# Performance work log

Measured on AMD Instinct MI355X. Metric: run time of the kernel, lower is better.

Reference implementation:

```python
import jax, jax.numpy as jnp
import numpy as np

N_NODES = 100000
N_EDGES = 625000
D = 128
N_LAYERS = 10

def setup_inputs() -> dict:
    key = jax.random.key(0)
    ks = jax.random.split(key, 6)
    x = jax.random.normal(ks[0], (N_NODES, D), dtype=jnp.float32)
    edge_index = jax.random.randint(ks[1], (2, N_EDGES), 0, N_NODES, dtype=jnp.int32)
    # PyG SAGEConv params per layer: lin_l (aggregated msgs, with bias), lin_r (root, no bias)
    scale = 1.0 / np.sqrt(D)
    Wl = jax.random.normal(ks[2], (N_LAYERS, D, D), dtype=jnp.float32) * scale
    Wr = jax.random.normal(ks[3], (N_LAYERS, D, D), dtype=jnp.float32) * scale
    b = jax.random.normal(ks[4], (N_LAYERS, D), dtype=jnp.float32) * 0.01
    return {"x": x, "Wl": Wl, "Wr": Wr, "b": b, "edge_index": edge_index}

def reference(x, Wl, Wr, b, edge_index):
    src = edge_index[0]
    dst = edge_index[1]
    n = x.shape[0]
    # in-degree for mean aggregation (clamped to avoid div by zero)
    deg = jax.ops.segment_sum(jnp.ones(src.shape[0], x.dtype), dst, num_segments=n)
    deg = jnp.maximum(deg, 1.0)[:, None]
    n_layers = Wl.shape[0]
    for i in range(n_layers):
        # SAGEConv: out = lin_l(mean_{j in N(i)} x_j) + lin_r(x_i)
        agg = jax.ops.segment_sum(x[src], dst, num_segments=n) / deg
        x = agg @ Wl[i] + x @ Wr[i] + b[i]
        if i < n_layers - 1:
            x = jax.nn.relu(x)  # dropout is identity in eval mode
    return x
```

## Files before the change

### kernel.cpp

```cpp
#include <hip/hip_runtime.h>
#include <hip/hip_bf16.h>

#define N_NODES 100000
#define N_EDGES 625000
#define D 128
#define N_LAYERS 10
#define SCAN_BLOCKS 98

typedef __attribute__((ext_vector_type(8))) short bf16x8;
typedef __attribute__((ext_vector_type(4))) float floatx4;

static __device__ __forceinline__ ushort f2bf(float f) {
    uint u = __float_as_uint(f);
    u += 0x7fff + ((u >> 16) & 1);
    return (ushort)(u >> 16);
}
static __device__ __forceinline__ float bf2f(ushort h) {
    return __uint_as_float(((uint)h) << 16);
}
static __device__ __forceinline__ uint packbf(float lo, float hi) {
    return (uint)f2bf(lo) | ((uint)f2bf(hi) << 16);
}


__global__ void hist_kernel(const int* __restrict__ dst, int* __restrict__ deg) {
    int e = blockIdx.x * blockDim.x + threadIdx.x;
    if (e < N_EDGES) atomicAdd(&deg[dst[e]], 1);
}

__global__ void scanA_kernel(const int* __restrict__ deg, int* __restrict__ offsets,
                             int* __restrict__ blockSums) {
    __shared__ int s[1024];
    int tid = threadIdx.x;
    int i = blockIdx.x * 1024 + tid;
    int v = (i < N_NODES) ? deg[i] : 0;
    s[tid] = v;
    __syncthreads();
    for (int d = 1; d < 1024; d <<= 1) {
        int t = (tid >= d) ? s[tid - d] : 0;
        __syncthreads();
        s[tid] += t;
        __syncthreads();
    }
    if (i < N_NODES) offsets[i] = s[tid] - v;
    if (tid == 1023) blockSums[blockIdx.x] = s[1023];
}

__global__ void scanB_kernel(const int* __restrict__ blockSums, int* __restrict__ blockOffsets) {
    __shared__ int s[128];
    int tid = threadIdx.x;
    int v = (tid < SCAN_BLOCKS) ? blockSums[tid] : 0;
    s[tid] = v;
    __syncthreads();
    for (int d = 1; d < 128; d <<= 1) {
        int t = (tid >= d) ? s[tid - d] : 0;
        __syncthreads();
        s[tid] += t;
        __syncthreads();
    }
    blockOffsets[tid] = s[tid] - v;
}

__global__ void scanC_kernel(int* __restrict__ offsets, const int* __restrict__ blockOffsets) {
    int i = blockIdx.x * 1024 + threadIdx.x;
    if (i < N_NODES) offsets[i] += blockOffsets[blockIdx.x];
}

__global__ void invdeg_kernel(const int* __restrict__ deg, float* __restrict__ invdeg,
                              int* __restrict__ offsets) {
    int i = blockIdx.x * blockDim.x + threadIdx.x;
    if (i < N_NODES) {
        int d = deg[i];
        invdeg[i] = 1.0f / (float)(d > 0 ? d : 1);
    }
    if (i == 0) offsets[N_NODES] = N_EDGES;
}

__global__ void scatter_kernel(const int* __restrict__ src, const int* __restrict__ dst,
                               const int* __restrict__ offsets, int* __restrict__ fill,
                               int* __restrict__ srcSorted) {
    int e = blockIdx.x * blockDim.x + threadIdx.x;
    if (e < N_EDGES) {
        int d_ = dst[e];
        int pos = offsets[d_] + atomicAdd(&fill[d_], 1);
        srcSorted[pos] = src[e];
    }
}

__global__ void wsplit_kernel(const float* __restrict__ Wl, const float* __restrict__ Wr,
                              ushort* __restrict__ Whi, ushort* __restrict__ Wlo) {
    int t = blockIdx.x * blockDim.x + threadIdx.x;
    if (t >= N_LAYERS * 4 * 16 * 64) return;
    int lane  = t & 63;
    int ntile = (t >> 6) & 15;
    int s     = (t >> 10) & 3;
    int layer = t >> 12;
    int n = ntile * 16 + (lane & 15);
    int kbase = s * 32 + (lane >> 4) * 8;
    const float* W = (n < 128) ? (Wl + (size_t)layer * D * D + n)
                               : (Wr + (size_t)layer * D * D + (n - 128));
    size_t off = (size_t)t * 8;
#pragma unroll
    for (int j = 0; j < 8; ++j) {
        float w = W[(size_t)(kbase + j) * D];
        ushort hh = f2bf(w);
        Whi[off + j] = hh;
        Wlo[off + j] = f2bf(w - bf2f(hh));
    }
}

static __device__ __forceinline__ int ntmap(int wave, int nt) {
    int base = (wave < 2) ? wave * 2 : 8 + (wave - 2) * 2;
    return base + (nt & 1) + ((nt >> 1) << 2);
}

__global__ __launch_bounds__(256) void gemm_hz(
        const float* __restrict__ X, const ushort* __restrict__ Whi,
        const ushort* __restrict__ Wlo, const float* __restrict__ bias,
        uint* __restrict__ h2out, uint* __restrict__ z2out) {
    __shared__ ushort Ahi[2][4 * 64 * 8];
    __shared__ ushort Alo[2][4 * 64 * 8];

    int tid  = threadIdx.x;
    int lane = tid & 63;
    int wave = tid >> 6;

    int r    = tid >> 4;
    int t0   = tid & 15;
    int s_st = t0 >> 2;
    int q_st = t0 & 3;
    int lanep = (q_st << 4) | r;
    int stIdx = (s_st * 64 + (lanep ^ (s_st << 2))) * 8;

    int q  = lane >> 4;
    int cc = lane & 15;

    int ntileMap[4];
#pragma unroll
    for (int nt = 0; nt < 4; ++nt) ntileMap[nt] = ntmap(wave, nt);

    float blo[2] = {0.f, 0.f}, bhi[2] = {0.f, 0.f};
    if (wave >= 2) {
#pragma unroll
        for (int p = 0; p < 2; ++p) {
            int c = (wave - 2) * 32 + p * 16 + cc;
            blo[p] = bias[c];
            bhi[p] = bias[c + 64];
        }
    }

    int row0 = blockIdx.x * 32;
#pragma unroll
    for (int st = 0; st < 2; ++st) {
        const float* xp = X + (size_t)(row0 + st * 16 + r) * D + t0 * 8;
        float4 v0 = *(const float4*)xp;
        float4 v1 = *(const float4*)(xp + 4);
        float a[8] = {v0.x, v0.y, v0.z, v0.w, v1.x, v1.y, v1.z, v1.w};
        ushort hi8[8], lo8[8];
#pragma unroll
        for (int j = 0; j < 8; ++j) {
            ushort hh = f2bf(a[j]);
            hi8[j] = hh;
            lo8[j] = f2bf(a[j] - bf2f(hh));
        }
        *(bf16x8*)&Ahi[st][stIdx] = *(bf16x8*)hi8;
        *(bf16x8*)&Alo[st][stIdx] = *(bf16x8*)lo8;
    }
    __syncthreads();

    floatx4 acc0[4], acc1[4];
#pragma unroll
    for (int nt = 0; nt < 4; ++nt) {
        acc0[nt] = (floatx4){0.f, 0.f, 0.f, 0.f};
        acc1[nt] = (floatx4){0.f, 0.f, 0.f, 0.f};
    }
#pragma unroll
    for (int s = 0; s < 4; ++s) {
        int aIdx = (s * 64 + (lane ^ (s << 2))) * 8;
        bf16x8 ah0 = *(const bf16x8*)&Ahi[0][aIdx];
        bf16x8 al0 = *(const bf16x8*)&Alo[0][aIdx];
        bf16x8 ah1 = *(const bf16x8*)&Ahi[1][aIdx];
        bf16x8 al1 = *(const bf16x8*)&Alo[1][aIdx];
#pragma unroll
        for (int nt = 0; nt < 4; ++nt) {
            size_t wo = ((size_t)(s * 16 + ntileMap[nt]) * 64 + lane) * 8;
            bf16x8 wh = *(const bf16x8*)&Whi[wo];
            bf16x8 wl = *(const bf16x8*)&Wlo[wo];
            acc0[nt] = __builtin_amdgcn_mfma_f32_16x16x32_bf16(ah0, wh, acc0[nt], 0, 0, 0);
            acc0[nt] = __builtin_amdgcn_mfma_f32_16x16x32_bf16(al0, wh, acc0[nt], 0, 0, 0);
            acc0[nt] = __builtin_amdgcn_mfma_f32_16x16x32_bf16(ah0, wl, acc0[nt], 0, 0, 0);
            acc1[nt] = __builtin_amdgcn_mfma_f32_16x16x32_bf16(ah1, wh, acc1[nt], 0, 0, 0);
            acc1[nt] = __builtin_amdgcn_mfma_f32_16x16x32_bf16(al1, wh, acc1[nt], 0, 0, 0);
            acc1[nt] = __builtin_amdgcn_mfma_f32_16x16x32_bf16(ah1, wl, acc1[nt], 0, 0, 0);
        }
    }

#pragma unroll
    for (int st = 0; st < 2; ++st) {
        floatx4* acc = st ? acc1 : acc0;
        int rowb = row0 + st * 16;
#pragma unroll
        for (int p = 0; p < 2; ++p) {
            if (wave < 2) {
                int c = wave * 32 + p * 16 + cc;
#pragma unroll
                for (int rr = 0; rr < 4; ++rr)
                    h2out[(size_t)(rowb + q * 4 + rr) * 64 + c] =
                        packbf(acc[p][rr], acc[p + 2][rr]);
            } else {
                int c = (wave - 2) * 32 + p * 16 + cc;
#pragma unroll
                for (int rr = 0; rr < 4; ++rr)
                    z2out[(size_t)(rowb + q * 4 + rr) * 64 + c] =
                        packbf(acc[p][rr] + blo[p], acc[p + 2][rr] + bhi[p]);
            }
        }
    }
}

static __device__ __forceinline__ void frag_write1(ushort* __restrict__ A,
                                                   int m, int c, float v) {
    int s_ = c >> 5, q_ = (c >> 3) & 3, j_ = c & 7;
    A[(s_ * 64 + (((q_ << 4) | m) ^ (s_ << 2))) * 8 + j_] = f2bf(v);
}

__global__ __launch_bounds__(256) void fused_layer(
        const uint* __restrict__ h2in, const int* __restrict__ srcSorted,
        const int* __restrict__ offsets, const float* __restrict__ invdeg,
        uint* __restrict__ z2io, const ushort* __restrict__ Whi,
        const ushort* __restrict__ Wlo, const float* __restrict__ bias,
        uint* __restrict__ h2out) {
    __shared__ ushort Ahi[4][4 * 64 * 8];

    int tid  = threadIdx.x;
    int lane = tid & 63;
    int wave = tid >> 6;
    int row0 = blockIdx.x * 64;

    int n0 = row0 + wave * 16;
    int offv = offsets[min(n0 + min(lane, 16), N_NODES)];
    float invv = invdeg[min(n0 + min(lane, 15), N_NODES - 1)];
    ushort* Afrag = Ahi[wave];

#pragma unroll
    for (int g = 0; g < 2; ++g) {
        int base = g * 8;
        int offG0 = __shfl(offv, base, 64);
        int totalG = __shfl(offv, base + 8, 64) - offG0;
        int idxv = srcSorted[min(offG0 + ((lane < totalG) ? lane : 0), N_EDGES - 1)];
        uint zG[8];
#pragma unroll
        for (int i = 0; i < 8; ++i)
            zG[i] = z2io[(size_t)min(n0 + base + i, N_NODES - 1) * 64 + lane];

        for (int i = 0; i < 8; ++i) {
            int sRel = __shfl(offv, base + i, 64) - offG0;
            int eRel = __shfl(offv, base + i + 1, 64) - offG0;
            int cnt = eRel - sRel;
            float sx = 0.f, sy = 0.f;
            if (cnt > 0 && eRel <= 64) {
                for (int k = sRel; k < eRel; k += 8) {
                    int sidx[8];
#pragma unroll
                    for (int j = 0; j < 8; ++j) {
                        int kk = k + j;
                        sidx[j] = __shfl(idxv, (kk < eRel) ? kk : sRel, 64);
                    }
                    uint u[8];
#pragma unroll
                    for (int j = 0; j < 8; ++j)
                        u[j] = h2in[(size_t)sidx[j] * 64 + lane];
#pragma unroll
                    for (int j = 0; j < 8; ++j) {
                        float m = ((k + j) < eRel) ? 1.f : 0.f;
                        sx += m * __uint_as_float(u[j] << 16);
                        sy += m * __uint_as_float(u[j] & 0xffff0000u);
                    }
                }
            } else if (cnt > 0) {
                int offn = offG0 + sRel;
                int nv = cnt < 64 ? cnt : 64;
                int idxn = srcSorted[offn + ((lane < nv) ? lane : 0)];
                for (int k = 0; k < nv; k += 8) {
                    int sidx[8];
#pragma unroll
                    for (int j = 0; j < 8; ++j) {
                        int kk = k + j;
                        sidx[j] = __shfl(idxn, (kk < nv) ? kk : 0, 64);
                    }
                    uint u[8];
#pragma unroll
                    for (int j = 0; j < 8; ++j)
                        u[j] = h2in[(size_t)sidx[j] * 64 + lane];
#pragma unroll
                    for (int j = 0; j < 8; ++j) {
                        float m = ((k + j) < nv) ? 1.f : 0.f;
                        sx += m * __uint_as_float(u[j] << 16);
                        sy += m * __uint_as_float(u[j] & 0xffff0000u);
                    }
                }
                for (int k = 64; k < cnt; ++k) {
                    int s = srcSorted[offn + k];
                    uint u = h2in[(size_t)s * 64 + lane];
                    sx += __uint_as_float(u << 16);
                    sy += __uint_as_float(u & 0xffff0000u);
                }
            }
            float inv = __shfl(invv, base + i, 64);
            uint zp = zG[i];
            float ox = fmaxf(sx * inv + __uint_as_float(zp << 16), 0.f);
            float oy = fmaxf(sy * inv + __uint_as_float(zp & 0xffff0000u), 0.f);
            int m = base + i;
            frag_write1(Afrag, m, lane, ox);
            frag_write1(Afrag, m, lane + 64, oy);
        }
    }
    __syncthreads();

    int q  = lane >> 4;
    int cc = lane & 15;
    int ntileMap[4];
#pragma unroll
    for (int nt = 0; nt < 4; ++nt) ntileMap[nt] = ntmap(wave, nt);

    float blo[2] = {0.f, 0.f}, bhi[2] = {0.f, 0.f};
    if (wave >= 2) {
#pragma unroll
        for (int p = 0; p < 2; ++p) {
            int c = (wave - 2) * 32 + p * 16 + cc;
            blo[p] = bias[c];
            bhi[p] = bias[c + 64];
        }
    }

    floatx4 acc[4][4];
#pragma unroll
    for (int st = 0; st < 4; ++st)
#pragma unroll
        for (int nt = 0; nt < 4; ++nt) acc[st][nt] = (floatx4){0.f, 0.f, 0.f, 0.f};

#pragma unroll
    for (int s = 0; s < 4; ++s) {
        int aIdx = (s * 64 + (lane ^ (s << 2))) * 8;
        bf16x8 a[4];
#pragma unroll
        for (int st = 0; st < 4; ++st) a[st] = *(const bf16x8*)&Ahi[st][aIdx];
#pragma unroll
        for (int nt = 0; nt < 4; ++nt) {
            size_t wo = ((size_t)(s * 16 + ntileMap[nt]) * 64 + lane) * 8;
            bf16x8 wh = *(const bf16x8*)&Whi[wo];
            bf16x8 wl = *(const bf16x8*)&Wlo[wo];
#pragma unroll
            for (int st = 0; st < 4; ++st) {
                acc[st][nt] = __builtin_amdgcn_mfma_f32_16x16x32_bf16(a[st], wh, acc[st][nt], 0, 0, 0);
                acc[st][nt] = __builtin_amdgcn_mfma_f32_16x16x32_bf16(a[st], wl, acc[st][nt], 0, 0, 0);
            }
        }
    }

#pragma unroll
    for (int st = 0; st < 4; ++st) {
        int rowb = row0 + st * 16;
#pragma unroll
        for (int p = 0; p < 2; ++p) {
            if (wave < 2) {
                int c = wave * 32 + p * 16 + cc;
#pragma unroll
                for (int rr = 0; rr < 4; ++rr) {
                    int row = rowb + q * 4 + rr;
                    if (row < N_NODES)
                        h2out[(size_t)row * 64 + c] = packbf(acc[st][p][rr], acc[st][p + 2][rr]);
                }
            } else {
                int c = (wave - 2) * 32 + p * 16 + cc;
#pragma unroll
                for (int rr = 0; rr < 4; ++rr) {
                    int row = rowb + q * 4 + rr;
                    if (row < N_NODES)
                        z2io[(size_t)row * 64 + c] =
                            packbf(acc[st][p][rr] + blo[p], acc[st][p + 2][rr] + bhi[p]);
                }
            }
        }
    }
}

__global__ __launch_bounds__(256) void agg_add_kernel(
        const uint* __restrict__ h2, const int* __restrict__ srcSorted,
        const int* __restrict__ offsets, const int* __restrict__ deg,
        const float* __restrict__ invdeg, const uint* __restrict__ z2,
        float* __restrict__ out) {
    int node = blockIdx.x * 4 + (threadIdx.x >> 6);
    int lane = threadIdx.x & 63;
    int off = offsets[node];
    int cnt = deg[node];
    float sx = 0.f, sy = 0.f;
    if (cnt > 0) {
        int nv = cnt < 64 ? cnt : 64;
        int idxv = srcSorted[off + ((lane < nv) ? lane : 0)];
        for (int k = 0; k < nv; k += 8) {
            int sidx[8];
#pragma unroll
            for (int j = 0; j < 8; ++j) {
                int kk = k + j;
                sidx[j] = __shfl(idxv, (kk < nv) ? kk : 0, 64);
            }
            uint u[8];
#pragma unroll
            for (int j = 0; j < 8; ++j)
                u[j] = h2[(size_t)sidx[j] * 64 + lane];
#pragma unroll
            for (int j = 0; j < 8; ++j) {
                float m = ((k + j) < nv) ? 1.f : 0.f;
                sx += m * __uint_as_float(u[j] << 16);
                sy += m * __uint_as_float(u[j] & 0xffff0000u);
            }
        }
        for (int k = 64; k < cnt; ++k) {
            int s = srcSorted[off + k];
            uint u = h2[(size_t)s * 64 + lane];
            sx += __uint_as_float(u << 16);
            sy += __uint_as_float(u & 0xffff0000u);
        }
    }
    float inv = invdeg[node];
    uint zp = z2[(size_t)node * 64 + lane];
    out[(size_t)node * 128 + lane]      = sx * inv + __uint_as_float(zp << 16);
    out[(size_t)node * 128 + 64 + lane] = sy * inv + __uint_as_float(zp & 0xffff0000u);
}

extern "C" void kernel_launch(void* const* d_in, const int* in_sizes, int n_in,
                              void* d_out, int out_size, void* d_ws, size_t ws_size,
                              hipStream_t stream) {
    const float* x  = (const float*)d_in[0];
    const float* Wl = (const float*)d_in[1];
    const float* Wr = (const float*)d_in[2];
    const float* b  = (const float*)d_in[3];
    const int*   ei = (const int*)d_in[4];
    const int* src = ei;
    const int* dst = ei + N_EDGES;
    float* out = (float*)d_out;

    char* w = (char*)d_ws;
    auto alloc = [&](size_t bytes) -> char* {
        char* p = w;
        w += (bytes + 255) & ~(size_t)255;
        return p;
    };
    uint*   z2        = (uint*)alloc((size_t)N_NODES * 64 * 4);
    uint*   hbufA     = (uint*)alloc((size_t)N_NODES * 64 * 4);
    uint*   hbufB     = (uint*)alloc((size_t)N_NODES * 64 * 4);
    ushort* Whi       = (ushort*)alloc((size_t)N_LAYERS * 4 * 16 * 64 * 8 * 2);
    ushort* Wlo       = (ushort*)alloc((size_t)N_LAYERS * 4 * 16 * 64 * 8 * 2);
    int*    deg       = (int*)alloc((size_t)N_NODES * 4);
    int*    offsets   = (int*)alloc((size_t)(N_NODES + 1) * 4);
    int*    fill      = (int*)alloc((size_t)N_NODES * 4);
    int*    srcSorted = (int*)alloc((size_t)N_EDGES * 4);
    int*    blockSums = (int*)alloc(128 * 4);
    int*    blockOffs = (int*)alloc(128 * 4);
    float*  invdeg    = (float*)alloc((size_t)N_NODES * 4);

    hipMemsetAsync(deg, 0, (size_t)N_NODES * 4, stream);
    hipMemsetAsync(fill, 0, (size_t)N_NODES * 4, stream);

    hist_kernel<<<(N_EDGES + 255) / 256, 256, 0, stream>>>(dst, deg);
    scanA_kernel<<<SCAN_BLOCKS, 1024, 0, stream>>>(deg, offsets, blockSums);
    scanB_kernel<<<1, 128, 0, stream>>>(blockSums, blockOffs);
    scanC_kernel<<<SCAN_BLOCKS, 1024, 0, stream>>>(offsets, blockOffs);
    invdeg_kernel<<<(N_NODES + 255) / 256, 256, 0, stream>>>(deg, invdeg, offsets);
    scatter_kernel<<<(N_EDGES + 255) / 256, 256, 0, stream>>>(src, dst, offsets, fill, srcSorted);
    wsplit_kernel<<<(N_LAYERS * 4 * 16 * 64 + 255) / 256, 256, 0, stream>>>(Wl, Wr, Whi, Wlo);

    gemm_hz<<<N_NODES / 32, 256, 0, stream>>>(x, Whi, Wlo, b, hbufA, z2);
    uint* hin = hbufA;
    uint* hout = hbufB;
    for (int L = 1; L < N_LAYERS; ++L) {
        size_t woff = (size_t)L * 4 * 16 * 64 * 8;
        fused_layer<<<(N_NODES + 63) / 64, 256, 0, stream>>>(
            hin, srcSorted, offsets, invdeg, z2,
            Whi + woff, Wlo + woff, b + (size_t)L * D, hout);
        uint* t = hin; hin = hout; hout = t;
    }
    agg_add_kernel<<<N_NODES / 4, 256, 0, stream>>>(
        hin, srcSorted, offsets, deg, invdeg, z2, out);
}
```

Baseline: 879.4 us.

## Shrink fused layer tile to 32 nodes per block with 8 nodes per wave

Each fused_layer block now handles 32 nodes instead of 64, with every wave aggregating 8 nodes rather than two groups of 8. This halves LDS and accumulator usage and doubles the grid size, aiming at more resident waves and better latency hiding on the gather. Bounds checks are dropped because N_NODES divides evenly by 32. The cost is that each block loads weight fragments for half as many rows, so weight reuse per MFMA drops.

```diff
diff --git a/kernel.cpp b/kernel.cpp
--- a/kernel.cpp
+++ b/kernel.cpp
@@ -230,90 +230,82 @@
         uint* __restrict__ z2io, const ushort* __restrict__ Whi,
         const ushort* __restrict__ Wlo, const float* __restrict__ bias,
         uint* __restrict__ h2out) {
-    __shared__ ushort Ahi[4][4 * 64 * 8];
+    __shared__ ushort Ahi[2][4 * 64 * 8];
 
     int tid  = threadIdx.x;
     int lane = tid & 63;
     int wave = tid >> 6;
-    int row0 = blockIdx.x * 64;
-
-    int n0 = row0 + wave * 16;
-    int offv = offsets[min(n0 + min(lane, 16), N_NODES)];
-    float invv = invdeg[min(n0 + min(lane, 15), N_NODES - 1)];
-    ushort* Afrag = Ahi[wave];
-
-#pragma unroll
-    for (int g = 0; g < 2; ++g) {
-        int base = g * 8;
-        int offG0 = __shfl(offv, base, 64);
-        int totalG = __shfl(offv, base + 8, 64) - offG0;
-        int idxv = srcSorted[min(offG0 + ((lane < totalG) ? lane : 0), N_EDGES - 1)];
-        uint zG[8];
-#pragma unroll
-        for (int i = 0; i < 8; ++i)
-            zG[i] = z2io[(size_t)min(n0 + base + i, N_NODES - 1) * 64 + lane];
-
-        for (int i = 0; i < 8; ++i) {
-            int sRel = __shfl(offv, base + i, 64) - offG0;
-            int eRel = __shfl(offv, base + i + 1, 64) - offG0;
-            int cnt = eRel - sRel;
-            float sx = 0.f, sy = 0.f;
-            if (cnt > 0 && eRel <= 64) {
-                for (int k = sRel; k < eRel; k += 8) {
-                    int sidx[8];
-#pragma unroll
-                    for (int j = 0; j < 8; ++j) {
-                        int kk = k + j;
-                        sidx[j] = __shfl(idxv, (kk < eRel) ? kk : sRel, 64);
-                    }
-                    uint u[8];
-#pragma unroll
-                    for (int j = 0; j < 8; ++j)
-                        u[j] = h2in[(size_t)sidx[j] * 64 + lane];
-#pragma unroll
-                    for (int j = 0; j < 8; ++j) {
-                        float m = ((k + j) < eRel) ? 1.f : 0.f;
-                        sx += m * __uint_as_float(u[j] << 16);
-                        sy += m * __uint_as_float(u[j] & 0xffff0000u);
-                    }
+    int row0 = blockIdx.x * 32;
+
+    int n0 = row0 + wave * 8;
+    int offv = offsets[n0 + min(lane, 8)];
+    float invv = invdeg[n0 + min(lane, 7)];
+    int off0 = __shfl(offv, 0, 64);
+    int total = __shfl(offv, 8, 64) - off0;
+    int idxv = srcSorted[min(off0 + ((lane < total) ? lane : 0), N_EDGES - 1)];
+    ushort* Afrag = Ahi[wave >> 1];
+
+    for (int i = 0; i < 8; ++i) {
+        int node = n0 + i;
+        int sRel = __shfl(offv, i, 64) - off0;
+        int eRel = __shfl(offv, i + 1, 64) - off0;
+        int cnt = eRel - sRel;
+        uint zp = z2io[(size_t)node * 64 + lane];
+        float sx = 0.f, sy = 0.f;
+        if (cnt > 0 && eRel <= 64) {
+            for (int k = sRel; k < eRel; k += 8) {
+                int sidx[8];
+#pragma unroll
+                for (int j = 0; j < 8; ++j) {
+                    int kk = k + j;
+                    sidx[j] = __shfl(idxv, (kk < eRel) ? kk : sRel, 64);
                 }
-            } else if (cnt > 0) {
-                int offn = offG0 + sRel;
-                int nv = cnt < 64 ? cnt : 64;
-                int idxn = srcSorted[offn + ((lane < nv) ? lane : 0)];
-                for (int k = 0; k < nv; k += 8) {
-                    int sidx[8];
-#pragma unroll
-                    for (int j = 0; j < 8; ++j) {
-                        int kk = k + j;
-                        sidx[j] = __shfl(idxn, (kk < nv) ? kk : 0, 64);
-                    }
-                    uint u[8];
-#pragma unroll
-                    for (int j = 0; j < 8; ++j)
-                        u[j] = h2in[(size_t)sidx[j] * 64 + lane];
-#pragma unroll
-                    for (int j = 0; j < 8; ++j) {
-                        float m = ((k + j) < nv) ? 1.f : 0.f;
-                        sx += m * __uint_as_float(u[j] << 16);
-                        sy += m * __uint_as_float(u[j] & 0xffff0000u);
-                    }
+                uint u[8];
+#pragma unroll
+                for (int j = 0; j < 8; ++j)
+                    u[j] = h2in[(size_t)sidx[j] * 64 + lane];
+#pragma unroll
+                for (int j = 0; j < 8; ++j) {
+                    float m = ((k + j) < eRel) ? 1.f : 0.f;
+                    sx += m * __uint_as_float(u[j] << 16);
+                    sy += m * __uint_as_float(u[j] & 0xffff0000u);
                 }
-                for (int k = 64; k < cnt; ++k) {
-                    int s = srcSorted[offn + k];
-                    uint u = h2in[(size_t)s * 64 + lane];
-                    sx += __uint_as_float(u << 16);
-                    sy += __uint_as_float(u & 0xffff0000u);
+            }
+        } else if (cnt > 0) {
+            int offn = off0 + sRel;
+            int nv = cnt < 64 ? cnt : 64;
+            int idxn = srcSorted[offn + ((lane < nv) ? lane : 0)];
+            for (int k = 0; k < nv; k += 8) {
+                int sidx[8];
+#pragma unroll
+                for (int j = 0; j < 8; ++j) {
+                    int kk = k + j;
+                    sidx[j] = __shfl(idxn, (kk < nv) ? kk : 0, 64);
                 }
-            }
-            float inv = __shfl(invv, base + i, 64);
-            uint zp = zG[i];
-            float ox = fmaxf(sx * inv + __uint_as_float(zp << 16), 0.f);
-            float oy = fmaxf(sy * inv + __uint_as_float(zp & 0xffff0000u), 0.f);
-            int m = base + i;
-            frag_write1(Afrag, m, lane, ox);
-            frag_write1(Afrag, m, lane + 64, oy);
-        }
+                uint u[8];
+#pragma unroll
+                for (int j = 0; j < 8; ++j)
+                    u[j] = h2in[(size_t)sidx[j] * 64 + lane];
+#pragma unroll
+                for (int j = 0; j < 8; ++j) {
+                    float m = ((k + j) < nv) ? 1.f : 0.f;
+                    sx += m * __uint_as_float(u[j] << 16);
+                    sy += m * __uint_as_float(u[j] & 0xffff0000u);
+                }
+            }
+            for (int k = 64; k < cnt; ++k) {
+                int s = srcSorted[offn + k];
+                uint u = h2in[(size_t)s * 64 + lane];
+                sx += __uint_as_float(u << 16);
+                sy += __uint_as_float(u & 0xffff0000u);
+            }
+        }
+        float inv = __shfl(invv, i, 64);
+        float ox = fmaxf(sx * inv + __uint_as_float(zp << 16), 0.f);
+        float oy = fmaxf(sy * inv + __uint_as_float(zp & 0xffff0000u), 0.f);
+        int m = (wave & 1) * 8 + i;
+        frag_write1(Afrag, m, lane, ox);
+        frag_write1(Afrag, m, lane + 64, oy);
     }
     __syncthreads();
 
@@ -333,53 +325,46 @@
         }
     }
 
-    floatx4 acc[4][4];
-#pragma unroll
-    for (int st = 0; st < 4; ++st)
+    floatx4 acc[2][4];
+#pragma unroll
+    for (int st = 0; st < 2; ++st)
 #pragma unroll
         for (int nt = 0; nt < 4; ++nt) acc[st][nt] = (floatx4){0.f, 0.f, 0.f, 0.f};
 
 #pragma unroll
     for (int s = 0; s < 4; ++s) {
         int aIdx = (s * 64 + (lane ^ (s << 2))) * 8;
-        bf16x8 a[4];
-#pragma unroll
-        for (int st = 0; st < 4; ++st) a[st] = *(const bf16x8*)&Ahi[st][aIdx];
+        bf16x8 a0 = *(const bf16x8*)&Ahi[0][aIdx];
+        bf16x8 a1 = *(const bf16x8*)&Ahi[1][aIdx];
 #pragma unroll
         for (int nt = 0; nt < 4; ++nt) {
             size_t wo = ((size_t)(s * 16 + ntileMap[nt]) * 64 + lane) * 8;
             bf16x8 wh = *(const bf16x8*)&Whi[wo];
             bf16x8 wl = *(const bf16x8*)&Wlo[wo];
-#pragma unroll
-            for (int st = 0; st < 4; ++st) {
-                acc[st][nt] = __builtin_amdgcn_mfma_f32_16x16x32_bf16(a[st], wh, acc[st][nt], 0, 0, 0);
-                acc[st][nt] = __builtin_amdgcn_mfma_f32_16x16x32_bf16(a[st], wl, acc[st][nt], 0, 0, 0);
-            }
-        }
-    }
-
-#pragma unroll
-    for (int st = 0; st < 4; ++st) {
+            acc[0][nt] = __builtin_amdgcn_mfma_f32_16x16x32_bf16(a0, wh, acc[0][nt], 0, 0, 0);
+            acc[0][nt] = __builtin_amdgcn_mfma_f32_16x16x32_bf16(a0, wl, acc[0][nt], 0, 0, 0);
+            acc[1][nt] = __builtin_amdgcn_mfma_f32_16x16x32_bf16(a1, wh, acc[1][nt], 0, 0, 0);
+            acc[1][nt] = __builtin_amdgcn_mfma_f32_16x16x32_bf16(a1, wl, acc[1][nt], 0, 0, 0);
+        }
+    }
+
+#pragma unroll
+    for (int st = 0; st < 2; ++st) {
         int rowb = row0 + st * 16;
 #pragma unroll
         for (int p = 0; p < 2; ++p) {
             if (wave < 2) {
                 int c = wave * 32 + p * 16 + cc;
 #pragma unroll
-                for (int rr = 0; rr < 4; ++rr) {
-                    int row = rowb + q * 4 + rr;
-                    if (row < N_NODES)
-                        h2out[(size_t)row * 64 + c] = packbf(acc[st][p][rr], acc[st][p + 2][rr]);
-                }
+                for (int rr = 0; rr < 4; ++rr)
+                    h2out[(size_t)(rowb + q * 4 + rr) * 64 + c] =
+                        packbf(acc[st][p][rr], acc[st][p + 2][rr]);
             } else {
                 int c = (wave - 2) * 32 + p * 16 + cc;
 #pragma unroll
-                for (int rr = 0; rr < 4; ++rr) {
-                    int row = rowb + q * 4 + rr;
-                    if (row < N_NODES)
-                        z2io[(size_t)row * 64 + c] =
-                            packbf(acc[st][p][rr] + blo[p], acc[st][p + 2][rr] + bhi[p]);
-                }
+                for (int rr = 0; rr < 4; ++rr)
+                    z2io[(size_t)(rowb + q * 4 + rr) * 64 + c] =
+                        packbf(acc[st][p][rr] + blo[p], acc[st][p + 2][rr] + bhi[p]);
             }
         }
     }
@@ -476,7 +461,7 @@
     uint* hout = hbufB;
     for (int L = 1; L < N_LAYERS; ++L) {
         size_t woff = (size_t)L * 4 * 16 * 64 * 8;
-        fused_layer<<<(N_NODES + 63) / 64, 256, 0, stream>>>(
+        fused_layer<<<N_NODES / 32, 256, 0, stream>>>(
             hin, srcSorted, offsets, invdeg, z2,
             Whi + woff, Wlo + woff, b + (size_t)L * D, hout);
         uint* t = hin; hin = hout; hout = t;
```

New measurement: 751.8 us. 14.5% less time.
